# Kernel optimization log

Measured on AMD Instinct MI355X. Metric: run time of the kernel, lower is better.

## Reference

```python
import jax, jax.numpy as jnp
import numpy as np

EPS = 1e-12  # F.normalize eps

def _normalize(v, axis):
    n = jnp.sqrt(jnp.sum(v * v, axis=axis, keepdims=True))
    return v / jnp.maximum(n, EPS)

def setup_inputs() -> dict:
    key = jax.random.key(0)
    ks = jax.random.split(key, 7)
    N, D, E = 100000, 128, 1600000
    x = jax.random.normal(ks[0], (N, D), dtype=jnp.float32)
    edge_index = jax.random.randint(ks[1], (2, E), 0, N, dtype=jnp.int64)
    s = 1.0 / np.sqrt(D)
    W_l = jax.random.normal(ks[2], (D, D), dtype=jnp.float32) * s
    b_l = jnp.zeros((D,), dtype=jnp.float32)
    W_r = jax.random.normal(ks[3], (D, D), dtype=jnp.float32) * s
    W1 = jax.random.normal(ks[4], (D, 10), dtype=jnp.float32)
    W2 = jax.random.normal(ks[5], (D, 20), dtype=jnp.float32)
    return {"x": x, "edge_index": edge_index, "W_l": W_l, "b_l": b_l,
            "W_r": W_r, "W1": W1, "W2": W2}

def reference(x, edge_index, W_l, b_l, W_r, W1, W2):
    N = x.shape[0]
    src, dst = edge_index[0], edge_index[1]
    # SAGEConv mean aggregation: gather source feats, scatter-mean to targets
    msg = x[src]                                   # [E, D]
    agg = jax.ops.segment_sum(msg, dst, num_segments=N)     # [N, D]
    deg = jax.ops.segment_sum(jnp.ones_like(dst, dtype=x.dtype), dst,
                              num_segments=N)               # [N]
    agg = agg / jnp.maximum(deg, 1.0)[:, None]
    # out = lin_l(agg) + lin_r(x)
    h = agg @ W_l + b_l + x @ W_r                  # [N, D]
    # NormedLinear heads: 10 * norm(h, dim=1) @ norm(W, dim=0)
    hn = _normalize(h, axis=1)
    out1 = 10.0 * (hn @ _normalize(W1, axis=0))
    out2 = 10.0 * (hn @ _normalize(W2, axis=0))
    return (out1, out2, h)
```

## Files before the change

kernel.cpp:

```cpp
#include <hip/hip_runtime.h>
#include <math.h>


typedef __attribute__((ext_vector_type(8))) short s16x8;
typedef __attribute__((ext_vector_type(4))) float f32x4;

#define NBLK 256
#define BLKT 512
#define SH 8
#define BMASK 255
#define CAP 64

static __device__ __forceinline__ unsigned short f2b(float f) {
  unsigned u = __builtin_bit_cast(unsigned, f);
  u += 0x7fff + ((u >> 16) & 1);
  return (unsigned short)(u >> 16);
}
static __device__ __forceinline__ float b2f(unsigned short s) {
  unsigned u = ((unsigned)s) << 16;
  return __builtin_bit_cast(float, u);
}


__global__ __launch_bounds__(BLKT) void scatter_direct(
    const int* __restrict__ ei, int* __restrict__ ebufC,
    int* __restrict__ cellcnt, int* __restrict__ tot,
    int E, int nb, int CH)
{
  __shared__ int cur[512];
  const int b = blockIdx.x;
  const int t = threadIdx.x;
  for (int i = t; i < nb; i += BLKT) cur[i] = 0;
  __syncthreads();
  const int e0 = b * CH, e1 = min(E, e0 + CH);
  const size_t base = (size_t)b * nb;
  for (int e = e0 + t; e < e1; e += BLKT) {
    int src = ei[e];
    int dst = ei[(size_t)E + e];
    int k = dst >> SH;
    int pos = atomicAdd(&cur[k], 1);
    if (pos < CAP)
      ebufC[(base + k) * CAP + pos] = (src << SH) | (dst & BMASK);
  }
  __syncthreads();
  for (int i = t; i < nb; i += BLKT) {
    int c = min(cur[i], CAP);
    cellcnt[base + i] = c;
    if (c) atomicAdd(&tot[i], c);
  }
}

__global__ __launch_bounds__(256) void bucket_scan(
    int* __restrict__ bstart, int nb, int E)
{
  __shared__ int s_sum[256];
  const int t = threadIdx.x;
  const int base = t * 2;
  int v0 = (base < nb) ? bstart[base] : 0;
  int v1 = (base + 1 < nb) ? bstart[base + 1] : 0;
  int s = v0 + v1;
  s_sum[t] = s;
  __syncthreads();
#pragma unroll
  for (int off = 1; off < 256; off <<= 1) {
    int add = (t >= off) ? s_sum[t - off] : 0;
    __syncthreads();
    s_sum[t] += add;
    __syncthreads();
  }
  int run = s_sum[t] - s;
  if (base < nb) bstart[base] = run;
  if (base + 1 < nb) bstart[base + 1] = run + v0;
  if (t == 255) bstart[nb] = E;
}

__global__ __launch_bounds__(256) void csr_finalize_direct(
    const int* __restrict__ ebufC, const int* __restrict__ cellcnt,
    const int* __restrict__ bstart,
    int* __restrict__ offs, int* __restrict__ elist, int N, int E, int nb)
{
  __shared__ int ncnt[256];
  __shared__ int sc[256];
  __shared__ int ncur[256];
  const int k = blockIdx.x;
  const int t = threadIdx.x;
  const int e0 = bstart[k];

  ncnt[t] = 0;
  __syncthreads();
  const int c = cellcnt[(size_t)t * nb + k];
  const int* cell = &ebufC[((size_t)t * nb + k) * CAP];
  for (int i = 0; i < c; ++i)
    atomicAdd(&ncnt[cell[i] & BMASK], 1);
  __syncthreads();
  int v = ncnt[t];
  sc[t] = v;
  __syncthreads();
#pragma unroll
  for (int off = 1; off < 256; off <<= 1) {
    int add = (t >= off) ? sc[t - off] : 0;
    __syncthreads();
    sc[t] += add;
    __syncthreads();
  }
  int ex = e0 + sc[t] - v;
  int node = (k << SH) + t;
  if (node < N) offs[node] = ex;
  ncur[t] = ex;
  if (k == 0 && t == 0) offs[N] = E;
  __syncthreads();
  for (int i = 0; i < c; ++i) {
    int w = cell[i];
    int pos = atomicAdd(&ncur[w & BMASK], 1);
    elist[pos] = w >> SH;
  }
}


__global__ __launch_bounds__(256) void conv_x_kernel(
    const float* __restrict__ x, short* __restrict__ hs, int n8,
    const float* __restrict__ Wl, const float* __restrict__ Wr,
    short* __restrict__ wbT, int* __restrict__ bstart, int nbp1)
{
  const int b = blockIdx.x;
  if (b < 2048) {
    const int stride = 2048 * 256;
    for (int i = b * 256 + threadIdx.x; i < n8; i += stride) {
      int row = i >> 4, seg = i & 15;
      float4 v0 = ((const float4*)x)[(size_t)row * 32 + seg * 2];
      float4 v1 = ((const float4*)x)[(size_t)row * 32 + seg * 2 + 1];
      s16x8 o;
      o[0] = (short)f2b(v0.x); o[1] = (short)f2b(v0.y);
      o[2] = (short)f2b(v0.z); o[3] = (short)f2b(v0.w);
      o[4] = (short)f2b(v1.x); o[5] = (short)f2b(v1.y);
      o[6] = (short)f2b(v1.z); o[7] = (short)f2b(v1.w);
      *(s16x8*)&hs[(size_t)row * 256 + seg * 8] = o;
    }
  } else if (b < 2064) {
    int i0 = (b - 2048) * 2048 + threadIdx.x;
#pragma unroll
    for (int u = 0; u < 8; ++u) {
      int i = i0 + u * 256;
      int c = i >> 8;
      int k = i & 255;
      float v = (k < 128) ? Wr[(size_t)k * 128 + c]
                          : Wl[(size_t)(k - 128) * 128 + c];
      wbT[i] = (short)f2b(v);
    }
  } else {
    for (int i = threadIdx.x; i < nbp1; i += 256) bstart[i] = 0;
  }
}


__global__ __launch_bounds__(256) void agg_gather_b(
    const short* __restrict__ hs_in, short* __restrict__ hs_out,
    const int* __restrict__ offs, const int* __restrict__ elist, int N)
{
  const int lane = threadIdx.x & 63;
  const int row = blockIdx.x * 4 + (threadIdx.x >> 6);
  if (row >= N) return;
  const int qt = lane >> 4;
  const int c  = lane & 15;
  const int start = offs[row], end = offs[row + 1];
  float a[8] = {0.f, 0.f, 0.f, 0.f, 0.f, 0.f, 0.f, 0.f};

  int j = start + qt;
  s16x8 v0 = {0, 0, 0, 0, 0, 0, 0, 0};
  if (j < end)
    v0 = *(const s16x8*)&hs_in[(size_t)elist[j] * 256 + c * 8];
  while (j < end) {
    int j1 = j + 4;
    s16x8 v1 = {0, 0, 0, 0, 0, 0, 0, 0};
    if (j1 < end)
      v1 = *(const s16x8*)&hs_in[(size_t)elist[j1] * 256 + c * 8];
#pragma unroll
    for (int k = 0; k < 8; ++k) a[k] += b2f((unsigned short)v0[k]);
    v0 = v1;
    j = j1;
  }
#pragma unroll
  for (int k = 0; k < 8; ++k) {
    a[k] += __shfl_xor(a[k], 16);
    a[k] += __shfl_xor(a[k], 32);
  }
  if (qt == 0) {
    float rd = 1.0f / fmaxf((float)(end - start), 1.0f);
    s16x8 o;
#pragma unroll
    for (int k = 0; k < 8; ++k) o[k] = (short)f2b(a[k] * rd);
    *(s16x8*)&hs_out[(size_t)row * 256 + 128 + c * 8] = o;
  }
}


__global__ __launch_bounds__(256, 4) void gemm_mfma(
    const short* __restrict__ hs, const short* __restrict__ wbT,
    const float* __restrict__ bl, float* __restrict__ h, int N)
{
  __shared__ short A_s[128][72];
  __shared__ short B_s[128][72];

  const int t = threadIdx.x;
  const int lane = t & 63;
  const int wid = t >> 6;
  const int wr = wid >> 1;
  const int wc = wid & 1;
  const int row0 = blockIdx.x * 128;
  const int l15 = lane & 15;
  const int lhi = lane >> 4;

  f32x4 acc[4][4];
#pragma unroll
  for (int m = 0; m < 4; ++m)
#pragma unroll
    for (int n = 0; n < 4; ++n) acc[m][n] = (f32x4){0.f, 0.f, 0.f, 0.f};

  for (int kc = 0; kc < 4; ++kc) {
    __syncthreads();
#pragma unroll
    for (int uu = 0; uu < 4; ++uu) {
      int u = t + uu * 256;
      int r = u >> 3;
      int s = u & 7;
      s16x8 va = {0, 0, 0, 0, 0, 0, 0, 0};
      int grow = row0 + r;
      if (grow < N)
        va = *(const s16x8*)&hs[(size_t)grow * 256 + kc * 64 + s * 8];
      *(s16x8*)&A_s[r][s * 8] = va;
      s16x8 vb = *(const s16x8*)&wbT[(size_t)r * 256 + kc * 64 + s * 8];
      *(s16x8*)&B_s[r][s * 8] = vb;
    }
    __syncthreads();

#pragma unroll
    for (int ks = 0; ks < 64; ks += 32) {
      const int klo = ks + lhi * 8;
      s16x8 af[4], bf[4];
#pragma unroll
      for (int m = 0; m < 4; ++m)
        af[m] = *(const s16x8*)&A_s[wr * 64 + m * 16 + l15][klo];
#pragma unroll
      for (int n = 0; n < 4; ++n)
        bf[n] = *(const s16x8*)&B_s[wc * 64 + n * 16 + l15][klo];
#pragma unroll
      for (int m = 0; m < 4; ++m)
#pragma unroll
        for (int n = 0; n < 4; ++n)
          acc[m][n] = __builtin_amdgcn_mfma_f32_16x16x32_bf16(
              af[m], bf[n], acc[m][n], 0, 0, 0);
    }
  }

  float bcol[4];
#pragma unroll
  for (int n = 0; n < 4; ++n) bcol[n] = bl[wc * 64 + n * 16 + l15];
#pragma unroll
  for (int m = 0; m < 4; ++m) {
    int grow_base = row0 + wr * 64 + m * 16 + lhi * 4;
#pragma unroll
    for (int r = 0; r < 4; ++r) {
      int grow = grow_base + r;
      if (grow < N) {
#pragma unroll
        for (int n = 0; n < 4; ++n) {
          int col = wc * 64 + n * 16 + l15;
          h[(size_t)grow * 128 + col] = acc[m][n][r] + bcol[n];
        }
      }
    }
  }
}


__global__ __launch_bounds__(256) void head_kernel(
    const float* __restrict__ h, const float* __restrict__ W1,
    const float* __restrict__ W2,
    float* __restrict__ out1, float* __restrict__ out2,
    int N, int c1, int c2)
{
  __shared__ float wc_s[30][132];
  __shared__ float wnorm[30];
  const int nc = c1 + c2;

  for (int i = threadIdx.x; i < nc * 128; i += 256) {
    int j = i >> 7, l = i & 127;
    wc_s[j][l] = (j < c1) ? W1[(size_t)l * c1 + j]
                          : W2[(size_t)l * c2 + (j - c1)];
  }
  __syncthreads();
  if (threadIdx.x < nc) {
    float ss = 0.f;
    for (int l = 0; l < 128; ++l) { float v = wc_s[threadIdx.x][l]; ss += v * v; }
    wnorm[threadIdx.x] = 1.0f / fmaxf(sqrtf(ss), 1e-12f);
  }
  __syncthreads();
  for (int i = threadIdx.x; i < nc * 128; i += 256) {
    int j = i >> 7;
    wc_s[j][i & 127] *= wnorm[j];
  }
  __syncthreads();

  int row = blockIdx.x * 256 + threadIdx.x;
  if (row >= N) return;
  const float4* h4 = (const float4*)(h + (size_t)row * 128);
  float acc[30];
#pragma unroll
  for (int j = 0; j < 30; ++j) acc[j] = 0.f;
  float ss = 0.f;
#pragma unroll 4
  for (int kk = 0; kk < 32; ++kk) {
    float4 v = h4[kk];
    ss += v.x * v.x + v.y * v.y + v.z * v.z + v.w * v.w;
#pragma unroll
    for (int j = 0; j < 30; ++j) {
      const float4 w = *(const float4*)&wc_s[j][kk * 4];
      acc[j] += v.x * w.x + v.y * w.y + v.z * w.z + v.w * w.w;
    }
  }
  float scale = 10.0f / fmaxf(sqrtf(ss), 1e-12f);
#pragma unroll
  for (int j = 0; j < 10; ++j) out1[(size_t)row * 10 + j] = scale * acc[j];
#pragma unroll
  for (int j = 0; j < 20; ++j) out2[(size_t)row * 20 + j] = scale * acc[10 + j];
}


__global__ __launch_bounds__(256) void edge_scatter(
    const float* __restrict__ x, const int* __restrict__ ei,
    float* __restrict__ agg, float* __restrict__ deg, int E)
{
  long long total = (long long)E * 32;
  long long stride = (long long)gridDim.x * blockDim.x;
  for (long long i = (long long)blockIdx.x * blockDim.x + threadIdx.x;
       i < total; i += stride) {
    int e = (int)(i >> 5);
    int c = (int)(i & 31);
    int src = ei[e];
    int dst = ei[(size_t)E + e];
    float4 v = ((const float4*)x)[(size_t)src * 32 + c];
    float* a = agg + (size_t)dst * 128 + c * 4;
    atomicAdd(a + 0, v.x);
    atomicAdd(a + 1, v.y);
    atomicAdd(a + 2, v.z);
    atomicAdd(a + 3, v.w);
    if (c == 0) atomicAdd(deg + dst, 1.0f);
  }
}

#define FMA4(accR, wv, s) { accR[0] += (s) * wv.x; accR[1] += (s) * wv.y; \
                            accR[2] += (s) * wv.z; accR[3] += (s) * wv.w; }

__global__ __launch_bounds__(256, 2) void gemm_h(
    const float* __restrict__ x, const float* __restrict__ Wl,
    const float* __restrict__ bl, const float* __restrict__ Wr,
    const float* __restrict__ degf, float* __restrict__ aggh, int N)
{
  __shared__ float a_s[128][36];
  __shared__ float x_s[128][36];
  __shared__ float wl_s[32][128];
  __shared__ float wr_s[32][128];

  const int t = threadIdx.x;
  const int tx = t & 15;
  const int ty = t >> 4;
  const int row0 = blockIdx.x * 128;

  float acc0[8][4];
  float acc1[8][4];
#pragma unroll
  for (int r = 0; r < 8; ++r)
#pragma unroll
    for (int c = 0; c < 4; ++c) { acc0[r][c] = 0.f; acc1[r][c] = 0.f; }

  for (int kc = 0; kc < 4; ++kc) {
    __syncthreads();
#pragma unroll
    for (int j = 0; j < 4; ++j) {
      int i = t + 256 * j;
      int r = i >> 3;
      int c4 = i & 7;
      int row = row0 + r;
      float4 av = {0.f, 0.f, 0.f, 0.f};
      float4 xv = {0.f, 0.f, 0.f, 0.f};
      if (row < N) {
        float rd = 1.0f / fmaxf(degf[row], 1.0f);
        av = ((const float4*)aggh)[(size_t)row * 32 + kc * 8 + c4];
        av.x *= rd; av.y *= rd; av.z *= rd; av.w *= rd;
        xv = ((const float4*)x)[(size_t)row * 32 + kc * 8 + c4];
      }
      *(float4*)&a_s[r][c4 * 4] = av;
      *(float4*)&x_s[r][c4 * 4] = xv;
    }
#pragma unroll
    for (int j = 0; j < 4; ++j) {
      int i = t + 256 * j;
      int kk = i >> 5;
      int c4 = i & 31;
      ((float4*)wl_s[kk])[c4] = ((const float4*)Wl)[(size_t)(kc * 32 + kk) * 32 + c4];
      ((float4*)wr_s[kk])[c4] = ((const float4*)Wr)[(size_t)(kc * 32 + kk) * 32 + c4];
    }
    __syncthreads();

#pragma unroll
    for (int k4 = 0; k4 < 8; ++k4) {
      float4 wl0[4], wl1[4], wr0[4], wr1[4];
#pragma unroll
      for (int kk = 0; kk < 4; ++kk) {
        int k = k4 * 4 + kk;
        wl0[kk] = *(const float4*)&wl_s[k][tx * 4];
        wl1[kk] = *(const float4*)&wl_s[k][64 + tx * 4];
        wr0[kk] = *(const float4*)&wr_s[k][tx * 4];
        wr1[kk] = *(const float4*)&wr_s[k][64 + tx * 4];
      }
#pragma unroll
      for (int r = 0; r < 8; ++r) {
        int rr = ty + 16 * r;
        float4 a  = *(const float4*)&a_s[rr][k4 * 4];
        float4 xv = *(const float4*)&x_s[rr][k4 * 4];
        FMA4(acc0[r], wl0[0], a.x); FMA4(acc0[r], wl0[1], a.y);
        FMA4(acc0[r], wl0[2], a.z); FMA4(acc0[r], wl0[3], a.w);
        FMA4(acc0[r], wr0[0], xv.x); FMA4(acc0[r], wr0[1], xv.y);
        FMA4(acc0[r], wr0[2], xv.z); FMA4(acc0[r], wr0[3], xv.w);
        FMA4(acc1[r], wl1[0], a.x); FMA4(acc1[r], wl1[1], a.y);
        FMA4(acc1[r], wl1[2], a.z); FMA4(acc1[r], wl1[3], a.w);
        FMA4(acc1[r], wr1[0], xv.x); FMA4(acc1[r], wr1[1], xv.y);
        FMA4(acc1[r], wr1[2], xv.z); FMA4(acc1[r], wr1[3], xv.w);
      }
    }
  }

  float4 b0 = ((const float4*)bl)[tx];
  float4 b1 = ((const float4*)bl)[16 + tx];
#pragma unroll
  for (int r = 0; r < 8; ++r) {
    int row = row0 + ty + 16 * r;
    if (row < N) {
      float4 o0 = { acc0[r][0] + b0.x, acc0[r][1] + b0.y,
                    acc0[r][2] + b0.z, acc0[r][3] + b0.w };
      float4 o1 = { acc1[r][0] + b1.x, acc1[r][1] + b1.y,
                    acc1[r][2] + b1.z, acc1[r][3] + b1.w };
      ((float4*)aggh)[(size_t)row * 32 + tx] = o0;
      ((float4*)aggh)[(size_t)row * 32 + 16 + tx] = o1;
    }
  }
}


extern "C" void kernel_launch(void* const* d_in, const int* in_sizes, int n_in,
                              void* d_out, int out_size, void* d_ws, size_t ws_size,
                              hipStream_t stream)
{
  const float* x  = (const float*)d_in[0];
  const int*   ei = (const int*)d_in[1];
  const float* Wl = (const float*)d_in[2];
  const float* bl = (const float*)d_in[3];
  const float* Wr = (const float*)d_in[4];
  const float* W1 = (const float*)d_in[5];
  const float* W2 = (const float*)d_in[6];

  const int N  = in_sizes[0] / 128;
  const int E  = in_sizes[1] / 2;
  const int c1 = in_sizes[5] / 128;
  const int c2 = in_sizes[6] / 128;
  const int nb = (N + 255) >> SH;
  const int CH = (E + NBLK - 1) / NBLK;

  float* out1 = (float*)d_out;
  float* out2 = out1 + (size_t)N * c1;
  float* h    = out2 + (size_t)N * c2;

  size_t ints = (size_t)NBLK * nb
              + (nb + 1)
              + (N + 1)
              + (size_t)E
              + (size_t)NBLK * nb * CAP;
  ints = (ints + 3) & ~(size_t)3;
  const size_t need = ints * sizeof(int)
                    + (size_t)128 * 256 * sizeof(short);

  if (ws_size >= need && nb <= 512 && CH / nb < CAP / 2) {
    int* cellcnt = (int*)d_ws;
    int* bstart  = cellcnt + (size_t)NBLK * nb;
    int* offs    = bstart + (nb + 1);
    int* elist   = offs + (N + 1);
    int* ebufC   = elist + E;
    short* wbT   = (short*)((int*)d_ws + ints);
    short* hs    = (short*)h;

    conv_x_kernel<<<2065, 256, 0, stream>>>(x, hs, N * 16, Wl, Wr, wbT,
                                            bstart, nb + 1);
    scatter_direct<<<NBLK, BLKT, 0, stream>>>(ei, ebufC, cellcnt, bstart, E, nb, CH);
    bucket_scan<<<1, 256, 0, stream>>>(bstart, nb, E);
    csr_finalize_direct<<<nb, 256, 0, stream>>>(ebufC, cellcnt, bstart,
                                                offs, elist, N, E, nb);
    agg_gather_b<<<(N + 3) / 4, 256, 0, stream>>>(hs, hs, offs, elist, N);
    gemm_mfma<<<(N + 127) / 128, 256, 0, stream>>>(hs, wbT, bl, h, N);
  } else {
    float* deg = out1;
    hipMemsetAsync(h,   0, (size_t)N * 128 * sizeof(float), stream);
    hipMemsetAsync(deg, 0, (size_t)N * sizeof(float), stream);
    edge_scatter<<<4096, 256, 0, stream>>>(x, ei, h, deg, E);
    gemm_h<<<(N + 127) / 128, 256, 0, stream>>>(x, Wl, bl, Wr, deg, h, N);
  }
  head_kernel<<<(N + 255) / 256, 256, 0, stream>>>(h, W1, W2, out1, out2, N, c1, c2);
}
```

Measured before the change: 172.5 us.

## Fuse edge bucketing with x/weight conversion and drop the separate bucket scan

Merges the x-to-bf16 conversion, weight transpose and edge bucket scatter into one heterogeneous launch, removing the bstart zeroing and the global atomic totals. The single-block bucket scan is replaced by each finalize block summing the earlier bucket counts directly from cellcnt. This removes two kernel launches and their serialization, but each finalize block now reads up to NBLK*k counts, which is redundant quadratic work across blocks. The GEMM launch bound also drops from 4 to 3 waves per SIMD, allowing more registers per thread.

```diff
diff --git a/kernel.cpp b/kernel.cpp
--- a/kernel.cpp
+++ b/kernel.cpp
@@ -22,110 +22,36 @@
 }
 
 
-__global__ __launch_bounds__(BLKT) void scatter_direct(
+__global__ __launch_bounds__(BLKT) void fused_pre(
     const int* __restrict__ ei, int* __restrict__ ebufC,
-    int* __restrict__ cellcnt, int* __restrict__ tot,
-    int E, int nb, int CH)
+    int* __restrict__ cellcnt, int E, int nb, int CH,
+    const float* __restrict__ x, short* __restrict__ hs, int n8,
+    const float* __restrict__ Wl, const float* __restrict__ Wr,
+    short* __restrict__ wbT)
 {
   __shared__ int cur[512];
   const int b = blockIdx.x;
   const int t = threadIdx.x;
-  for (int i = t; i < nb; i += BLKT) cur[i] = 0;
-  __syncthreads();
-  const int e0 = b * CH, e1 = min(E, e0 + CH);
-  const size_t base = (size_t)b * nb;
-  for (int e = e0 + t; e < e1; e += BLKT) {
-    int src = ei[e];
-    int dst = ei[(size_t)E + e];
-    int k = dst >> SH;
-    int pos = atomicAdd(&cur[k], 1);
-    if (pos < CAP)
-      ebufC[(base + k) * CAP + pos] = (src << SH) | (dst & BMASK);
-  }
-  __syncthreads();
-  for (int i = t; i < nb; i += BLKT) {
-    int c = min(cur[i], CAP);
-    cellcnt[base + i] = c;
-    if (c) atomicAdd(&tot[i], c);
-  }
-}
-
-__global__ __launch_bounds__(256) void bucket_scan(
-    int* __restrict__ bstart, int nb, int E)
-{
-  __shared__ int s_sum[256];
-  const int t = threadIdx.x;
-  const int base = t * 2;
-  int v0 = (base < nb) ? bstart[base] : 0;
-  int v1 = (base + 1 < nb) ? bstart[base + 1] : 0;
-  int s = v0 + v1;
-  s_sum[t] = s;
-  __syncthreads();
-#pragma unroll
-  for (int off = 1; off < 256; off <<= 1) {
-    int add = (t >= off) ? s_sum[t - off] : 0;
-    __syncthreads();
-    s_sum[t] += add;
-    __syncthreads();
-  }
-  int run = s_sum[t] - s;
-  if (base < nb) bstart[base] = run;
-  if (base + 1 < nb) bstart[base + 1] = run + v0;
-  if (t == 255) bstart[nb] = E;
-}
-
-__global__ __launch_bounds__(256) void csr_finalize_direct(
-    const int* __restrict__ ebufC, const int* __restrict__ cellcnt,
-    const int* __restrict__ bstart,
-    int* __restrict__ offs, int* __restrict__ elist, int N, int E, int nb)
-{
-  __shared__ int ncnt[256];
-  __shared__ int sc[256];
-  __shared__ int ncur[256];
-  const int k = blockIdx.x;
-  const int t = threadIdx.x;
-  const int e0 = bstart[k];
-
-  ncnt[t] = 0;
-  __syncthreads();
-  const int c = cellcnt[(size_t)t * nb + k];
-  const int* cell = &ebufC[((size_t)t * nb + k) * CAP];
-  for (int i = 0; i < c; ++i)
-    atomicAdd(&ncnt[cell[i] & BMASK], 1);
-  __syncthreads();
-  int v = ncnt[t];
-  sc[t] = v;
-  __syncthreads();
-#pragma unroll
-  for (int off = 1; off < 256; off <<= 1) {
-    int add = (t >= off) ? sc[t - off] : 0;
-    __syncthreads();
-    sc[t] += add;
-    __syncthreads();
-  }
-  int ex = e0 + sc[t] - v;
-  int node = (k << SH) + t;
-  if (node < N) offs[node] = ex;
-  ncur[t] = ex;
-  if (k == 0 && t == 0) offs[N] = E;
-  __syncthreads();
-  for (int i = 0; i < c; ++i) {
-    int w = cell[i];
-    int pos = atomicAdd(&ncur[w & BMASK], 1);
-    elist[pos] = w >> SH;
-  }
-}
-
-
-__global__ __launch_bounds__(256) void conv_x_kernel(
-    const float* __restrict__ x, short* __restrict__ hs, int n8,
-    const float* __restrict__ Wl, const float* __restrict__ Wr,
-    short* __restrict__ wbT, int* __restrict__ bstart, int nbp1)
-{
-  const int b = blockIdx.x;
-  if (b < 2048) {
-    const int stride = 2048 * 256;
-    for (int i = b * 256 + threadIdx.x; i < n8; i += stride) {
+
+  if (b < NBLK) {
+    for (int i = t; i < nb; i += BLKT) cur[i] = 0;
+    __syncthreads();
+    const int e0 = b * CH, e1 = min(E, e0 + CH);
+    const size_t base = (size_t)b * nb;
+    for (int e = e0 + t; e < e1; e += BLKT) {
+      int src = ei[e];
+      int dst = ei[(size_t)E + e];
+      int k = dst >> SH;
+      int pos = atomicAdd(&cur[k], 1);
+      if (pos < CAP)
+        ebufC[(base + k) * CAP + pos] = (src << SH) | (dst & BMASK);
+    }
+    __syncthreads();
+    for (int i = t; i < nb; i += BLKT)
+      cellcnt[base + i] = min(cur[i], CAP);
+  } else if (b < NBLK + 1024) {
+    const int stride = 1024 * BLKT;
+    for (int i = (b - NBLK) * BLKT + t; i < n8; i += stride) {
       int row = i >> 4, seg = i & 15;
       float4 v0 = ((const float4*)x)[(size_t)row * 32 + seg * 2];
       float4 v1 = ((const float4*)x)[(size_t)row * 32 + seg * 2 + 1];
@@ -136,19 +62,71 @@
       o[6] = (short)f2b(v1.z); o[7] = (short)f2b(v1.w);
       *(s16x8*)&hs[(size_t)row * 256 + seg * 8] = o;
     }
-  } else if (b < 2064) {
-    int i0 = (b - 2048) * 2048 + threadIdx.x;
-#pragma unroll
-    for (int u = 0; u < 8; ++u) {
-      int i = i0 + u * 256;
+  } else {
+    int i0 = (b - NBLK - 1024) * 2048 + t;
+#pragma unroll
+    for (int u = 0; u < 4; ++u) {
+      int i = i0 + u * 512;
       int c = i >> 8;
       int k = i & 255;
       float v = (k < 128) ? Wr[(size_t)k * 128 + c]
                           : Wl[(size_t)(k - 128) * 128 + c];
       wbT[i] = (short)f2b(v);
     }
-  } else {
-    for (int i = threadIdx.x; i < nbp1; i += 256) bstart[i] = 0;
+  }
+}
+
+
+__global__ __launch_bounds__(256) void csr_finalize_direct(
+    const int* __restrict__ ebufC, const int* __restrict__ cellcnt,
+    int* __restrict__ offs, int* __restrict__ elist, int N, int E, int nb)
+{
+  __shared__ int ncnt[256];
+  __shared__ int sc[256];
+  __shared__ int ncur[256];
+  __shared__ int wred[4];
+  __shared__ int e0sh;
+  const int k = blockIdx.x;
+  const int t = threadIdx.x;
+
+  int acc = 0;
+  for (int b = 0; b < NBLK; ++b)
+    for (int j = t; j < k; j += 256)
+      acc += cellcnt[(size_t)b * nb + j];
+#pragma unroll
+  for (int m = 1; m < 64; m <<= 1) acc += __shfl_xor(acc, m);
+  if ((t & 63) == 0) wred[t >> 6] = acc;
+  ncnt[t] = 0;
+  __syncthreads();
+  if (t == 0) e0sh = wred[0] + wred[1] + wred[2] + wred[3];
+  __syncthreads();
+  const int e0 = e0sh;
+
+  const int c = cellcnt[(size_t)t * nb + k];
+  const int* cell = &ebufC[((size_t)t * nb + k) * CAP];
+  for (int i = 0; i < c; ++i)
+    atomicAdd(&ncnt[cell[i] & BMASK], 1);
+  __syncthreads();
+  int v = ncnt[t];
+  sc[t] = v;
+  __syncthreads();
+#pragma unroll
+  for (int off = 1; off < 256; off <<= 1) {
+    int add = (t >= off) ? sc[t - off] : 0;
+    __syncthreads();
+    sc[t] += add;
+    __syncthreads();
+  }
+  int ex = e0 + sc[t] - v;
+  int node = (k << SH) + t;
+  if (node < N) offs[node] = ex;
+  ncur[t] = ex;
+  if (k == 0 && t == 0) offs[N] = E;
+  __syncthreads();
+  for (int i = 0; i < c; ++i) {
+    int w = cell[i];
+    int pos = atomicAdd(&ncur[w & BMASK], 1);
+    elist[pos] = w >> SH;
   }
 }
 
@@ -194,7 +172,7 @@
 }
 
 
-__global__ __launch_bounds__(256, 4) void gemm_mfma(
+__global__ __launch_bounds__(256, 3) void gemm_mfma(
     const short* __restrict__ hs, const short* __restrict__ wbT,
     const float* __restrict__ bl, float* __restrict__ h, int N)
 {
@@ -471,7 +449,6 @@
   float* h    = out2 + (size_t)N * c2;
 
   size_t ints = (size_t)NBLK * nb
-              + (nb + 1)
               + (N + 1)
               + (size_t)E
               + (size_t)NBLK * nb * CAP;
@@ -481,18 +458,15 @@
 
   if (ws_size >= need && nb <= 512 && CH / nb < CAP / 2) {
     int* cellcnt = (int*)d_ws;
-    int* bstart  = cellcnt + (size_t)NBLK * nb;
-    int* offs    = bstart + (nb + 1);
+    int* offs    = cellcnt + (size_t)NBLK * nb;
     int* elist   = offs + (N + 1);
     int* ebufC   = elist + E;
     short* wbT   = (short*)((int*)d_ws + ints);
     short* hs    = (short*)h;
 
-    conv_x_kernel<<<2065, 256, 0, stream>>>(x, hs, N * 16, Wl, Wr, wbT,
-                                            bstart, nb + 1);
-    scatter_direct<<<NBLK, BLKT, 0, stream>>>(ei, ebufC, cellcnt, bstart, E, nb, CH);
-    bucket_scan<<<1, 256, 0, stream>>>(bstart, nb, E);
-    csr_finalize_direct<<<nb, 256, 0, stream>>>(ebufC, cellcnt, bstart,
+    fused_pre<<<NBLK + 1024 + 16, BLKT, 0, stream>>>(
+        ei, ebufC, cellcnt, E, nb, CH, x, hs, N * 16, Wl, Wr, wbT);
+    csr_finalize_direct<<<nb, 256, 0, stream>>>(ebufC, cellcnt,
                                                 offs, elist, N, E, nb);
     agg_gather_b<<<(N + 3) / 4, 256, 0, stream>>>(hs, hs, offs, elist, N);
     gemm_mfma<<<(N + 127) / 128, 256, 0, stream>>>(hs, wbT, bl, h, N);
```

Result: slower. 267.4 us (+55.0%).
